# Kernel optimization log

Hardware: AMD Instinct MI355X
Metric: run time of the kernel (lower is better)

The kernel has to match this reference:

```python
import jax, jax.numpy as jnp
import numpy as np

FEATS = [(100, 100), (50, 50), (25, 25), (13, 13)]  # (W, H) per level
BS, NQ, D = 2, 10000, 256
NH, NL, NP, G = 8, 4, 4, 8
HD = D // NH


def grid_sample_bilinear(im, grid):
    """torch.nn.functional.grid_sample(mode='bilinear', padding_mode='zeros', align_corners=False).
    im: [N, C, H, W]; grid: [N, Hg, Wg, 2] in [-1, 1] (x, y). Returns [N, C, Hg, Wg]."""
    N, C, H, W = im.shape
    Hg, Wg = grid.shape[1], grid.shape[2]
    x = (grid[..., 0] + 1.0) * (W * 0.5) - 0.5
    y = (grid[..., 1] + 1.0) * (H * 0.5) - 0.5
    x0 = jnp.floor(x); y0 = jnp.floor(y)
    wx1 = x - x0; wx0 = 1.0 - wx1
    wy1 = y - y0; wy0 = 1.0 - wy1
    imf = im.reshape(N, C, H * W)

    def corner(xi, yi, w):
        inb = (xi >= 0) & (xi < W) & (yi >= 0) & (yi < H)
        xi_c = jnp.clip(xi, 0, W - 1).astype(jnp.int32)
        yi_c = jnp.clip(yi, 0, H - 1).astype(jnp.int32)
        idx = (yi_c * W + xi_c).reshape(N, 1, Hg * Wg)
        vals = jnp.take_along_axis(imf, idx, axis=2).reshape(N, C, Hg, Wg)
        return vals * (w * inb.astype(im.dtype))[:, None]

    out = (corner(x0, y0, wx0 * wy0) + corner(x0 + 1, y0, wx1 * wy0)
           + corner(x0, y0 + 1, wx0 * wy1) + corner(x0 + 1, y0 + 1, wx1 * wy1))
    return out


def setup_inputs() -> dict:
    key = jax.random.key(0)
    ks = jax.random.split(key, 7)
    nv = sum(w * h for (w, h) in FEATS)
    return {
        "query": jax.random.normal(ks[0], (BS, NQ, D), jnp.float32),
        "value": jax.random.normal(ks[1], (BS, nv, NH, HD), jnp.float32),
        "reference_points": jax.random.uniform(ks[2], (BS, NQ, NL, 2), jnp.float32),
        "spatial_shapes": jnp.array(FEATS, jnp.float32),  # rows are (W, H)
        "W_off": jax.random.normal(ks[3], (NH * NL * NP * 2, D), jnp.float32) * 0.02,
        "b_off": jax.random.normal(ks[4], (NH * NL * NP * 2,), jnp.float32) * 0.5,
        "W_attn": jax.random.normal(ks[5], (NH * NL * NP, D), jnp.float32) * 0.02,
        "b_attn": jax.random.normal(ks[6], (NH * NL * NP,), jnp.float32) * 0.02,
    }


def reference(query, value, reference_points, spatial_shapes, W_off, b_off, W_attn, b_attn):
    bs, nq, _ = query.shape
    # sampling offsets: [bs, nq, NH, NL*NP*2] with (level, point, xy) layout
    off = (jnp.einsum('bqd,od->bqo', query, W_off) + b_off).reshape(bs, nq, NH, NL * NP * 2)
    # reference points tiled to the same (level, point, xy) layout
    ref = jnp.broadcast_to(reference_points[:, :, None, :, None, :],
                           (bs, nq, NH, NL, NP, 2)).reshape(bs, nq, NH, NL * NP * 2)
    # offset normalizer: (1/W, 1/H) per level, tiled over points
    inv = 1.0 / spatial_shapes  # [NL, 2]
    norm = jnp.broadcast_to(inv[:, None, :], (NL, NP, 2)).reshape(-1)
    loc = (ref + off * norm) * 2.0 - 1.0  # [bs, nq, NH, NL*NP*2]
    loc = loc.reshape(bs, nq, NH, NL, NP, 2)

    # attention weights: softmax over (NL*NP), then rearranged to [bs*NH, 1, nq/G, NL*G*NP]
    aw = jax.nn.softmax((jnp.einsum('bqd,od->bqo', query, W_attn) + b_attn)
                        .reshape(bs, nq, NH, NL * NP), axis=-1)
    aw = aw.reshape(bs, nq // G, G, NH, NL, NP).transpose(0, 3, 1, 4, 2, 5)
    aw = aw.reshape(bs * NH, 1, nq // G, NL * G * NP)

    # per-level grid_sample
    sizes = [w * h for (w, h) in FEATS]
    starts = np.concatenate([[0], np.cumsum(sizes)]).tolist()
    sampled = []
    for lvl, (Wl, Hl) in enumerate(FEATS):
        val_l = value[:, starts[lvl]:starts[lvl + 1]]  # [bs, Hl*Wl, NH, HD]
        val_l = val_l.transpose(0, 2, 3, 1).reshape(bs * NH, HD, Hl, Wl)
        grid_l = loc[:, :, :, lvl].transpose(0, 2, 1, 3, 4)  # [bs, NH, nq, NP, 2]
        grid_l = grid_l.reshape(bs * NH, nq // G, G * NP, 2)
        sampled.append(grid_sample_bilinear(val_l, grid_l))  # [bs*NH, HD, nq/G, G*NP]
    sv = jnp.concatenate(sampled, axis=-1)  # [bs*NH, HD, nq/G, NL*G*NP]

    out = sv * aw
    # reduce_sum linear (fixed 0/1 weight from init_weights) == sum over levels and points per group slot
    out = out.reshape(bs * NH, HD, nq // G, NL, G, NP).sum(axis=(3, 5))  # [bs*NH, HD, nq/G, G]
    return out.reshape(bs, NH * HD, nq)
```

## Files before the change

### kernel.cpp

```cpp
#include <hip/hip_runtime.h>

#define NQ   10000
#define BSZ  2
#define DIM  256
#define NH   8
#define HD   32
#define NLV  4
#define NPT  4
#define NV   13294
#define MT   (BSZ*NQ)
#define NOUT 384
#define NVAL (BSZ*NV*NH*HD)
#define GEMM_BLOCKS 939
#define PREP_BLOCKS 6647

typedef float    floatx4 __attribute__((ext_vector_type(4)));
typedef int      intx4   __attribute__((ext_vector_type(4)));
typedef __bf16   bf16x8  __attribute__((ext_vector_type(8)));
typedef _Float16 halfx8  __attribute__((ext_vector_type(8)));
typedef _Float16 halfx4  __attribute__((ext_vector_type(4)));

__device__ __forceinline__ unsigned pk_bf16(float lo, float hi) {
  return __builtin_amdgcn_perm(__float_as_uint(hi) + 0x8000u,
                               __float_as_uint(lo) + 0x8000u, 0x07060302);
}

__device__ __forceinline__ unsigned short f32_to_f16_bits(float f) {
  _Float16 h = (_Float16)f;
  return __builtin_bit_cast(unsigned short, h);
}

__global__ __launch_bounds__(256) void gp_kernel(
    const float* __restrict__ query, const float* __restrict__ W_off,
    const float* __restrict__ W_attn,
    const float* __restrict__ b_off, const float* __restrict__ b_attn,
    const float* __restrict__ value,
    _Float16* __restrict__ rawh, _Float16* __restrict__ vf16) {
  const int bid = blockIdx.x;
  const int tid = threadIdx.x;
  if (bid >= GEMM_BLOCKS) {
    int i = (bid - GEMM_BLOCKS) * 256 + tid;
    if (i * 4 < NVAL) {
      floatx4 v = *(const floatx4*)&value[i * 4];
      halfx4 t = { (_Float16)v.x, (_Float16)v.y, (_Float16)v.z, (_Float16)v.w };
      *(uint2*)&vf16[i * 4] = *(const uint2*)&t;
    }
    return;
  }
  __shared__ unsigned short As[64][40];
  __shared__ unsigned short Bs[128][40];
  const int n0 = (bid % 3) * 128;
  const int m0 = (bid / 3) * 64;
  const int wave = tid >> 6;
  const int lane = tid & 63;
  const int quad = lane >> 4;
  const int l16  = lane & 15;
  floatx4 acc[8] = {};
  const int ar = tid >> 2;
  const int ac = (tid & 3) * 8;
  const int br = tid >> 1;
  const int bc = (tid & 1) * 16;
  const float* __restrict__ Wsrc =
      (n0 < 256) ? (W_off + (size_t)n0 * DIM) : (W_attn + (size_t)(n0 - 256) * DIM);

  for (int k0 = 0; k0 < DIM; k0 += 32) {
    {
      int gm = m0 + ar;
      floatx4 a0 = {}, a1 = {};
      if (gm < MT) {
        const float* src = query + (size_t)gm * DIM + k0 + ac;
        a0 = *(const floatx4*)src;
        a1 = *(const floatx4*)(src + 4);
      }
      uint4 ua = { pk_bf16(a0.x, a0.y), pk_bf16(a0.z, a0.w),
                   pk_bf16(a1.x, a1.y), pk_bf16(a1.z, a1.w) };
      *(uint4*)&As[ar][ac] = ua;
    }
    {
      const float* src = Wsrc + (size_t)br * DIM + k0 + bc;
      floatx4 b0 = *(const floatx4*)src;
      floatx4 b1 = *(const floatx4*)(src + 4);
      floatx4 b2 = *(const floatx4*)(src + 8);
      floatx4 b3 = *(const floatx4*)(src + 12);
      uint4 u0 = { pk_bf16(b0.x, b0.y), pk_bf16(b0.z, b0.w),
                   pk_bf16(b1.x, b1.y), pk_bf16(b1.z, b1.w) };
      uint4 u1 = { pk_bf16(b2.x, b2.y), pk_bf16(b2.z, b2.w),
                   pk_bf16(b3.x, b3.y), pk_bf16(b3.z, b3.w) };
      *(uint4*)&Bs[br][bc]     = u0;
      *(uint4*)&Bs[br][bc + 8] = u1;
    }
    __syncthreads();
    bf16x8 a = *(const bf16x8*)&As[wave*16 + l16][quad*8];
    #pragma unroll
    for (int nt = 0; nt < 8; nt++) {
      bf16x8 b = *(const bf16x8*)&Bs[nt*16 + l16][quad*8];
      acc[nt] = __builtin_amdgcn_mfma_f32_16x16x32_bf16(a, b, acc[nt], 0, 0, 0);
    }
    __syncthreads();
  }
  #pragma unroll
  for (int nt = 0; nt < 8; nt++) {
    int gn = n0 + nt*16 + l16;
    float bias = (gn < 256) ? b_off[gn] : b_attn[gn - 256];
    #pragma unroll
    for (int r = 0; r < 4; r++) {
      int gm = m0 + wave*16 + quad*4 + r;
      if (gm < MT) rawh[(size_t)gm*NOUT + gn] = (_Float16)(acc[nt][r] + bias);
    }
  }
}

__global__ __launch_bounds__(256) void sample_kernel(
    const _Float16* __restrict__ rawh, const _Float16* __restrict__ vf16,
    const float* __restrict__ refp, _Float16* __restrict__ tmph) {
  const int b  = blockIdx.y;
  const int q0 = blockIdx.x * 8;
  const int mbase = b * NQ + q0;
  const int tid = threadIdx.x;

  __shared__ int          s_off[64 * 68];
  __shared__ unsigned int s_w  [64 * 34];
  __shared__ float        s_aw [64 * 17];

  const int WLI[4] = {100, 50, 25, 13};
  const int STI[4] = {0, 10000, 12500, 13125};

  float rpx[4], rpy[4];

  #pragma unroll
  for (int it = 0; it < 4; ++it) {
    int slot = it * 256 + tid;
    int ql = slot >> 7, r = slot & 127, h = r >> 4, lp = r & 15, l = lp >> 2, p = lp & 3;
    int m = mbase + ql;
    const _Float16* rp = rawh + (size_t)m * NOUT;
    float offx = (float)rp[h*32 + l*8 + p*2 + 0];
    float offy = (float)rp[h*32 + l*8 + p*2 + 1];
    s_aw[(ql*8 + h)*17 + lp] = (float)rp[256 + h*16 + lp];
    float Wl = (float)WLI[l];
    float rx = refp[(m*NLV + l)*2 + 0];
    float ry = refp[(m*NLV + l)*2 + 1];
    rpx[it] = rx * Wl + offx - 0.5f;
    rpy[it] = ry * Wl + offy - 0.5f;
  }
  __syncthreads();

  if (tid < 64) {
    int base = tid * 17;
    float mx = -1e30f;
    #pragma unroll
    for (int i = 0; i < 16; i++) mx = fmaxf(mx, s_aw[base + i]);
    float s = 0.f;
    float e[16];
    #pragma unroll
    for (int i = 0; i < 16; i++) { e[i] = expf(s_aw[base + i] - mx); s += e[i]; }
    float inv = 1.f / s;
    #pragma unroll
    for (int i = 0; i < 16; i++) s_aw[base + i] = e[i] * inv;
  }
  __syncthreads();

  #pragma unroll
  for (int it = 0; it < 4; ++it) {
    int slot = it * 256 + tid;
    int ql = slot >> 7, r = slot & 127, h = r >> 4, lp = r & 15, l = lp >> 2;
    int rowqh = ql*8 + h;
    float aw = s_aw[rowqh*17 + lp];
    float px = rpx[it], py = rpy[it];
    float x0f = floorf(px), y0f = floorf(py);
    int x0 = (int)x0f, y0 = (int)y0f;
    float wx1 = px - x0f, wx0 = 1.f - wx1;
    float wy1 = py - y0f, wy0 = 1.f - wy1;
    int Wl = WLI[l], STl = STI[l];
    int offs[4]; unsigned short wb[4];
    #pragma unroll
    for (int t = 0; t < 4; ++t) {
      int xi = x0 + (t & 1), yi = y0 + (t >> 1);
      bool inb = (xi >= 0) & (xi < Wl) & (yi >= 0) & (yi < Wl);
      offs[t] = inb ? ((STl + yi*Wl + xi) * 512 + h * 64) : 0;
      float w = inb ? (aw * ((t & 1) ? wx1 : wx0) * ((t >> 1) ? wy1 : wy0)) : 0.f;
      wb[t] = f32_to_f16_bits(w);
    }
    *(intx4*)&s_off[rowqh*68 + lp*4] = *(const intx4*)offs;
    uint2 wp = { (unsigned)wb[0] | ((unsigned)wb[1] << 16),
                 (unsigned)wb[2] | ((unsigned)wb[3] << 16) };
    *(uint2*)&s_w[rowqh*34 + lp*2] = wp;
  }
  __syncthreads();

  const int wv = tid >> 6, lane = tid & 63;
  const int qh = lane >> 5, ql = wv*2 + qh;
  const int h = (lane >> 2) & 7, cq = lane & 3;
  const char* vb = (const char*)vf16 + (size_t)b * (NV*NH*HD*2) + cq * 16;
  floatx4 acc0 = {0.f,0.f,0.f,0.f}, acc1 = {0.f,0.f,0.f,0.f};
  const int orow = (ql*8 + h) * 68, wrow = (ql*8 + h) * 34;
  #pragma unroll 4
  for (int pt = 0; pt < 16; ++pt) {
    intx4 offs = *(const intx4*)&s_off[orow + pt*4];
    uint2 wp   = *(const uint2*)&s_w[wrow + pt*2];
    halfx4 hw  = __builtin_bit_cast(halfx4, wp);
    halfx8 v0 = *(const halfx8*)(vb + offs.x);
    halfx8 v1 = *(const halfx8*)(vb + offs.y);
    halfx8 v2 = *(const halfx8*)(vb + offs.z);
    halfx8 v3 = *(const halfx8*)(vb + offs.w);
    #pragma unroll
    for (int t = 0; t < 4; ++t) {
      halfx8 v = (t==0) ? v0 : (t==1) ? v1 : (t==2) ? v2 : v3;
      float w = (float)hw[t];
      acc0.x += w * (float)v[0];
      acc0.y += w * (float)v[1];
      acc0.z += w * (float)v[2];
      acc0.w += w * (float)v[3];
      acc1.x += w * (float)v[4];
      acc1.y += w * (float)v[5];
      acc1.z += w * (float)v[6];
      acc1.w += w * (float)v[7];
    }
  }
  int m = mbase + ql;
  uint4 st = { __builtin_bit_cast(unsigned, __builtin_amdgcn_cvt_pkrtz(acc0.x, acc0.y)),
               __builtin_bit_cast(unsigned, __builtin_amdgcn_cvt_pkrtz(acc0.z, acc0.w)),
               __builtin_bit_cast(unsigned, __builtin_amdgcn_cvt_pkrtz(acc1.x, acc1.y)),
               __builtin_bit_cast(unsigned, __builtin_amdgcn_cvt_pkrtz(acc1.z, acc1.w)) };
  *(uint4*)&tmph[(size_t)m * DIM + h*HD + cq*8] = st;
}

__global__ __launch_bounds__(256) void transpose_kernel(
    const _Float16* __restrict__ tmph, float* __restrict__ out) {
  __shared__ float tile[32][33];
  const int b  = blockIdx.z;
  const int q0 = blockIdx.x * 32;
  const int c0 = blockIdx.y * 32;
  const int tx = threadIdx.x & 31;
  const int ty = threadIdx.x >> 5;
  #pragma unroll
  for (int i = 0; i < 4; i++) {
    int qq = q0 + ty + i*8;
    tile[ty + i*8][tx] = (qq < NQ) ? (float)tmph[((size_t)b*NQ + qq)*DIM + c0 + tx] : 0.f;
  }
  __syncthreads();
  if (q0 + tx < NQ) {
    #pragma unroll
    for (int i = 0; i < 4; i++) {
      out[((size_t)b*DIM + c0 + ty + i*8)*NQ + q0 + tx] = tile[tx][ty + i*8];
    }
  }
}

extern "C" void kernel_launch(void* const* d_in, const int* in_sizes, int n_in,
                              void* d_out, int out_size, void* d_ws, size_t ws_size,
                              hipStream_t stream) {
  const float* query  = (const float*)d_in[0];
  const float* value  = (const float*)d_in[1];
  const float* refp   = (const float*)d_in[2];
  const float* W_off  = (const float*)d_in[4];
  const float* b_off  = (const float*)d_in[5];
  const float* W_attn = (const float*)d_in[6];
  const float* b_attn = (const float*)d_in[7];
  float* out = (float*)d_out;

  char* ws = (char*)d_ws;
  _Float16* rawh = (_Float16*)ws;
  _Float16* tmph = (_Float16*)(ws + 15360000);
  _Float16* vf16 = (_Float16*)(ws + 25600000);

  hipLaunchKernelGGL(gp_kernel, dim3(GEMM_BLOCKS + PREP_BLOCKS), dim3(256), 0, stream,
                     query, W_off, W_attn, b_off, b_attn, value, rawh, vf16);
  hipLaunchKernelGGL(sample_kernel, dim3(NQ / 8, BSZ), dim3(256), 0, stream,
                     rawh, vf16, refp, tmph);
  hipLaunchKernelGGL(transpose_kernel, dim3(313, 8, 2), dim3(256), 0, stream,
                     tmph, out);
}
```

Baseline: 164.5 us.

## Compute softmax with wave shuffles and store 16-bit sample indices in LDS

The sampling kernel's prep phase is remapped so each thread handles one (query, head, point) across all four levels. The softmax over 16 logits is then computed in registers with xor-shuffles across 4 lanes, which removes the s_aw shared array, one __syncthreads and the serial 64-thread softmax. Corner offsets are stored in LDS as packed 16-bit pixel indices instead of 32-bit byte offsets, halving that LDS footprint, and the head offset moves into the base pointer. This adds shift/mask work in the gather loop and uses the faster __expf.

```diff
diff --git a/kernel.cpp b/kernel.cpp
--- a/kernel.cpp
+++ b/kernel.cpp
@@ -19,6 +19,7 @@
 typedef __bf16   bf16x8  __attribute__((ext_vector_type(8)));
 typedef _Float16 halfx8  __attribute__((ext_vector_type(8)));
 typedef _Float16 halfx4  __attribute__((ext_vector_type(4)));
+typedef _Float16 halfx2  __attribute__((ext_vector_type(2)));
 
 __device__ __forceinline__ unsigned pk_bf16(float lo, float hi) {
   return __builtin_amdgcn_perm(__float_as_uint(hi) + 0x8000u,
@@ -118,90 +119,89 @@
   const int mbase = b * NQ + q0;
   const int tid = threadIdx.x;
 
-  __shared__ int          s_off[64 * 68];
+  __shared__ unsigned int s_idx[64 * 34];
   __shared__ unsigned int s_w  [64 * 34];
-  __shared__ float        s_aw [64 * 17];
-
-  const int WLI[4] = {100, 50, 25, 13};
-  const int STI[4] = {0, 10000, 12500, 13125};
-
-  float rpx[4], rpy[4];
-
+
+  constexpr int WLI[4] = {100, 50, 25, 13};
+  constexpr int STI[4] = {0, 10000, 12500, 13125};
+
+  const int p   = tid & 3;
+  const int r   = tid >> 2;
+  const int hh  = r & 7;
+  const int ql0 = r >> 3;
+  const int m   = mbase + ql0;
+  const _Float16* rp = rawh + (size_t)m * NOUT;
+
+  float lg[4], rpx[4], rpy[4];
   #pragma unroll
   for (int it = 0; it < 4; ++it) {
-    int slot = it * 256 + tid;
-    int ql = slot >> 7, r = slot & 127, h = r >> 4, lp = r & 15, l = lp >> 2, p = lp & 3;
-    int m = mbase + ql;
-    const _Float16* rp = rawh + (size_t)m * NOUT;
-    float offx = (float)rp[h*32 + l*8 + p*2 + 0];
-    float offy = (float)rp[h*32 + l*8 + p*2 + 1];
-    s_aw[(ql*8 + h)*17 + lp] = (float)rp[256 + h*16 + lp];
-    float Wl = (float)WLI[l];
-    float rx = refp[(m*NLV + l)*2 + 0];
-    float ry = refp[(m*NLV + l)*2 + 1];
-    rpx[it] = rx * Wl + offx - 0.5f;
-    rpy[it] = ry * Wl + offy - 0.5f;
-  }
-  __syncthreads();
-
-  if (tid < 64) {
-    int base = tid * 17;
-    float mx = -1e30f;
-    #pragma unroll
-    for (int i = 0; i < 16; i++) mx = fmaxf(mx, s_aw[base + i]);
-    float s = 0.f;
-    float e[16];
-    #pragma unroll
-    for (int i = 0; i < 16; i++) { e[i] = expf(s_aw[base + i] - mx); s += e[i]; }
-    float inv = 1.f / s;
-    #pragma unroll
-    for (int i = 0; i < 16; i++) s_aw[base + i] = e[i] * inv;
-  }
-  __syncthreads();
+    unsigned oxy = *(const unsigned*)(rp + hh*32 + it*8 + p*2);
+    halfx2 o2 = __builtin_bit_cast(halfx2, oxy);
+    lg[it] = (float)rp[256 + hh*16 + it*4 + p];
+    float Wl = (float)WLI[it];
+    float rx = refp[((size_t)m*NLV + it)*2 + 0];
+    float ry = refp[((size_t)m*NLV + it)*2 + 1];
+    rpx[it] = rx * Wl + (float)o2.x - 0.5f;
+    rpy[it] = ry * Wl + (float)o2.y - 0.5f;
+  }
+
+  float mx = fmaxf(fmaxf(lg[0], lg[1]), fmaxf(lg[2], lg[3]));
+  mx = fmaxf(mx, __shfl_xor(mx, 1));
+  mx = fmaxf(mx, __shfl_xor(mx, 2));
+  float e[4], sden = 0.f;
+  #pragma unroll
+  for (int it = 0; it < 4; ++it) { e[it] = __expf(lg[it] - mx); sden += e[it]; }
+  sden += __shfl_xor(sden, 1);
+  sden += __shfl_xor(sden, 2);
+  float inv = 1.f / sden;
 
   #pragma unroll
   for (int it = 0; it < 4; ++it) {
-    int slot = it * 256 + tid;
-    int ql = slot >> 7, r = slot & 127, h = r >> 4, lp = r & 15, l = lp >> 2;
-    int rowqh = ql*8 + h;
-    float aw = s_aw[rowqh*17 + lp];
+    float aw = e[it] * inv;
     float px = rpx[it], py = rpy[it];
     float x0f = floorf(px), y0f = floorf(py);
     int x0 = (int)x0f, y0 = (int)y0f;
     float wx1 = px - x0f, wx0 = 1.f - wx1;
     float wy1 = py - y0f, wy0 = 1.f - wy1;
-    int Wl = WLI[l], STl = STI[l];
-    int offs[4]; unsigned short wb[4];
+    const int Wl = WLI[it], STl = STI[it];
+    unsigned short ib[4], wb[4];
     #pragma unroll
     for (int t = 0; t < 4; ++t) {
       int xi = x0 + (t & 1), yi = y0 + (t >> 1);
       bool inb = (xi >= 0) & (xi < Wl) & (yi >= 0) & (yi < Wl);
-      offs[t] = inb ? ((STl + yi*Wl + xi) * 512 + h * 64) : 0;
+      ib[t] = inb ? (unsigned short)(STl + yi*Wl + xi) : (unsigned short)0;
       float w = inb ? (aw * ((t & 1) ? wx1 : wx0) * ((t >> 1) ? wy1 : wy0)) : 0.f;
       wb[t] = f32_to_f16_bits(w);
     }
-    *(intx4*)&s_off[rowqh*68 + lp*4] = *(const intx4*)offs;
+    const int lp2 = (it*4 + p) * 2;
+    uint2 ip = { (unsigned)ib[0] | ((unsigned)ib[1] << 16),
+                 (unsigned)ib[2] | ((unsigned)ib[3] << 16) };
     uint2 wp = { (unsigned)wb[0] | ((unsigned)wb[1] << 16),
                  (unsigned)wb[2] | ((unsigned)wb[3] << 16) };
-    *(uint2*)&s_w[rowqh*34 + lp*2] = wp;
+    *(uint2*)&s_idx[r*34 + lp2] = ip;
+    *(uint2*)&s_w  [r*34 + lp2] = wp;
   }
   __syncthreads();
 
   const int wv = tid >> 6, lane = tid & 63;
   const int qh = lane >> 5, ql = wv*2 + qh;
   const int h = (lane >> 2) & 7, cq = lane & 3;
-  const char* vb = (const char*)vf16 + (size_t)b * (NV*NH*HD*2) + cq * 16;
+  const char* vbh = (const char*)vf16 + (size_t)b * (NV*NH*HD*2) + h*64 + cq*16;
   floatx4 acc0 = {0.f,0.f,0.f,0.f}, acc1 = {0.f,0.f,0.f,0.f};
-  const int orow = (ql*8 + h) * 68, wrow = (ql*8 + h) * 34;
+  const int row = (ql*8 + h) * 34;
   #pragma unroll 4
   for (int pt = 0; pt < 16; ++pt) {
-    intx4 offs = *(const intx4*)&s_off[orow + pt*4];
-    uint2 wp   = *(const uint2*)&s_w[wrow + pt*2];
-    halfx4 hw  = __builtin_bit_cast(halfx4, wp);
-    halfx8 v0 = *(const halfx8*)(vb + offs.x);
-    halfx8 v1 = *(const halfx8*)(vb + offs.y);
-    halfx8 v2 = *(const halfx8*)(vb + offs.z);
-    halfx8 v3 = *(const halfx8*)(vb + offs.w);
+    uint2 ui = *(const uint2*)&s_idx[row + pt*2];
+    uint2 wp = *(const uint2*)&s_w  [row + pt*2];
+    halfx4 hw = __builtin_bit_cast(halfx4, wp);
+    int o0 = (int)(ui.x & 0xffffu) << 9;
+    int o1 = (int)(ui.x >> 16)     << 9;
+    int o2 = (int)(ui.y & 0xffffu) << 9;
+    int o3 = (int)(ui.y >> 16)     << 9;
+    halfx8 v0 = *(const halfx8*)(vbh + o0);
+    halfx8 v1 = *(const halfx8*)(vbh + o1);
+    halfx8 v2 = *(const halfx8*)(vbh + o2);
+    halfx8 v3 = *(const halfx8*)(vbh + o3);
     #pragma unroll
     for (int t = 0; t < 4; ++t) {
       halfx8 v = (t==0) ? v0 : (t==1) ? v1 : (t==2) ? v2 : v3;
@@ -216,12 +216,12 @@
       acc1.w += w * (float)v[7];
     }
   }
-  int m = mbase + ql;
+  int mo = mbase + ql;
   uint4 st = { __builtin_bit_cast(unsigned, __builtin_amdgcn_cvt_pkrtz(acc0.x, acc0.y)),
                __builtin_bit_cast(unsigned, __builtin_amdgcn_cvt_pkrtz(acc0.z, acc0.w)),
                __builtin_bit_cast(unsigned, __builtin_amdgcn_cvt_pkrtz(acc1.x, acc1.y)),
                __builtin_bit_cast(unsigned, __builtin_amdgcn_cvt_pkrtz(acc1.z, acc1.w)) };
-  *(uint4*)&tmph[(size_t)m * DIM + h*HD + cq*8] = st;
+  *(uint4*)&tmph[(size_t)mo * DIM + h*HD + cq*8] = st;
 }
 
 __global__ __launch_bounds__(256) void transpose_kernel(
```

Measured after the change: 169.3 us. +2.9%, slower.
